# Kernel optimization log

Measured on AMD Instinct MI355X. Metric: run time of the kernel, lower is better.

## Reference

```python
import jax, jax.numpy as jnp
import numpy as np

L, H, N = 4096, 256, 64  # seq_len, hidden_size, hippo_n
EPS = 1e-5


def setup_inputs() -> dict:
    key = jax.random.key(0)
    ks = jax.random.split(key, 8)
    x = jax.random.normal(ks[0], (L, H), jnp.float32)
    # S4D-Lin style initialization for the diagonal SSM (H independent SSMs of state size N)
    Lambda_re = -0.5 * jnp.ones((H, N), jnp.float32)
    Lambda_im = jnp.tile(jnp.pi * jnp.arange(N, dtype=jnp.float32), (H, 1))
    B_re = jnp.ones((H, N), jnp.float32)
    B_im = jnp.zeros((H, N), jnp.float32)
    C_re = jax.random.normal(ks[1], (H, N), jnp.float32) * (0.5 ** 0.5)
    C_im = jax.random.normal(ks[2], (H, N), jnp.float32) * (0.5 ** 0.5)
    D = jax.random.normal(ks[3], (H,), jnp.float32)
    log_step = jax.random.uniform(ks[4], (H,), jnp.float32,
                                  minval=jnp.log(0.001), maxval=jnp.log(0.1))
    ln_w = jnp.ones((H,), jnp.float32)
    ln_b = jnp.zeros((H,), jnp.float32)
    sc = 1.0 / jnp.sqrt(jnp.float32(H))
    W1 = jax.random.normal(ks[5], (H, H), jnp.float32) * sc
    b1 = jnp.zeros((H,), jnp.float32)
    W2 = jax.random.normal(ks[6], (H, H), jnp.float32) * sc
    b2 = jnp.zeros((H,), jnp.float32)
    return {"x": x, "Lambda_re": Lambda_re, "Lambda_im": Lambda_im,
            "B_re": B_re, "B_im": B_im, "C_re": C_re, "C_im": C_im,
            "D": D, "log_step": log_step, "ln_w": ln_w, "ln_b": ln_b,
            "W1": W1, "b1": b1, "W2": W2, "b2": b2}


def reference(x, Lambda_re, Lambda_im, B_re, B_im, C_re, C_im, D, log_step,
              ln_w, ln_b, W1, b1, W2, b2):
    skip = x
    # per-token LayerNorm over the H feature axis (eqx.nn.LayerNorm, eps=1e-5)
    mu = jnp.mean(x, axis=-1, keepdims=True)
    var = jnp.mean(jnp.square(x - mu), axis=-1, keepdims=True)
    xn = (x - mu) / jnp.sqrt(var + EPS) * ln_w + ln_b  # [L, H]

    # ZOH discretization of the diagonal SSM (the cell.ssm(L) step)
    Lam = Lambda_re + 1j * Lambda_im                     # [H, N] complex64
    dt = jnp.exp(log_step)[:, None]                      # [H, 1]
    Ab = jnp.exp(Lam * dt)                               # [H, N]
    Bb = (Ab - 1.0) / Lam * (B_re + 1j * B_im)           # [H, N]
    C = C_re + 1j * C_im                                 # [H, N]

    def step(s, u):  # s: [H, N] complex state, u: [H] input at one time step
        s = Ab * s + Bb * u[:, None]
        y = 2.0 * jnp.einsum('hn,hn->h', C, s).real + D * u
        return s, y

    s0 = jnp.zeros((H, N), jnp.complex64)
    hidden, ys = jax.lax.scan(step, s0, xn)              # ys: [L, H]

    g = jax.nn.gelu(ys)
    out = (g @ W1.T + b1) * jax.nn.sigmoid(g @ W2.T + b2)  # GLU epilogue
    return (hidden, skip + out)
```

## Files before the change

### kernel.cpp

```cpp
#include <hip/hip_runtime.h>
#include <hip/hip_bf16.h>

#define LSEQ 4096
#define HDIM 256
#define NS   64
#define PC   32
#define MC   128

typedef __attribute__((ext_vector_type(8))) short short8;
typedef __attribute__((ext_vector_type(4))) float floatx4;

__global__ __launch_bounds__(256) void k_ln_stats(const float* __restrict__ x,
                                                  float* __restrict__ mu,
                                                  float* __restrict__ rstd) {
    int l = blockIdx.x, t = threadIdx.x;
    float v = x[l * HDIM + t];
    float s = v, s2 = v * v;
#pragma unroll
    for (int o = 32; o; o >>= 1) {
        s  += __shfl_xor(s, o);
        s2 += __shfl_xor(s2, o);
    }
    __shared__ float ps[4], ps2[4];
    int w = t >> 6;
    if ((t & 63) == 0) { ps[w] = s; ps2[w] = s2; }
    __syncthreads();
    if (t == 0) {
        float S = ps[0] + ps[1] + ps[2] + ps[3];
        float S2 = ps2[0] + ps2[1] + ps2[2] + ps2[3];
        float m = S * (1.0f / HDIM);
        float var = S2 * (1.0f / HDIM) - m * m;
        mu[l] = m;
        rstd[l] = rsqrtf(var + 1e-5f);
    }
}

__global__ __launch_bounds__(256) void k_transnorm(const float* __restrict__ x,
                                                   const float* __restrict__ mu,
                                                   const float* __restrict__ rstd,
                                                   const float* __restrict__ w,
                                                   const float* __restrict__ b,
                                                   float* __restrict__ xnT) {
    __shared__ float tile[64 * 65];
    int l0 = blockIdx.x * 64, h0 = blockIdx.y * 64;
    int t = threadIdx.x;
#pragma unroll
    for (int i = 0; i < 16; ++i) {
        int e = i * 256 + t;
        int r = e >> 6, c = e & 63;
        int l = l0 + r, h = h0 + c;
        float v = x[l * HDIM + h];
        v = (v - mu[l]) * rstd[l] * w[h] + b[h];
        tile[c * 65 + r] = v;
    }
    __syncthreads();
#pragma unroll
    for (int i = 0; i < 16; ++i) {
        int e = i * 256 + t;
        int hh = e >> 6, ll = e & 63;
        xnT[(size_t)(h0 + hh) * LSEQ + l0 + ll] = tile[hh * 65 + ll];
    }
}

__global__ __launch_bounds__(256) void k_wconv(const float* __restrict__ W1,
                                               const float* __restrict__ W2,
                                               unsigned short* __restrict__ w1b,
                                               unsigned short* __restrict__ w2b) {
    int g = blockIdx.x * 256 + threadIdx.x;
    float4 a = ((const float4*)W1)[g];
    float4 c = ((const float4*)W2)[g];
    ushort4 o1, o2;
    __hip_bfloat16 h;
    h = __float2bfloat16(a.x); o1.x = *(unsigned short*)&h;
    h = __float2bfloat16(a.y); o1.y = *(unsigned short*)&h;
    h = __float2bfloat16(a.z); o1.z = *(unsigned short*)&h;
    h = __float2bfloat16(a.w); o1.w = *(unsigned short*)&h;
    h = __float2bfloat16(c.x); o2.x = *(unsigned short*)&h;
    h = __float2bfloat16(c.y); o2.y = *(unsigned short*)&h;
    h = __float2bfloat16(c.z); o2.z = *(unsigned short*)&h;
    h = __float2bfloat16(c.w); o2.w = *(unsigned short*)&h;
    ((ushort4*)w1b)[g] = o1;
    ((ushort4*)w2b)[g] = o2;
}

__device__ inline void ssm_consts(const float* Lre, const float* Lim,
                                  const float* Bre, const float* Bim,
                                  const float* lstep, int h, int n,
                                  float& are, float& aim, float& bre, float& bim) {
    int idx = h * NS + n;
    float lre = Lre[idx], lim = Lim[idx];
    float dt = expf(lstep[h]);
    float er = expf(lre * dt);
    float sa, ca;
    sincosf(lim * dt, &sa, &ca);
    are = er * ca; aim = er * sa;
    float inv = 1.0f / (lre * lre + lim * lim);
    float nre = are - 1.0f, nim = aim;
    float tre = (nre * lre + nim * lim) * inv;
    float tim = (nim * lre - nre * lim) * inv;
    float br = Bre[idx], bi = Bim[idx];
    bre = tre * br - tim * bi;
    bim = tre * bi + tim * br;
}

__global__ __launch_bounds__(256) void k_scan_local(const float* __restrict__ xnT,
                                                    const float* __restrict__ Lre,
                                                    const float* __restrict__ Lim,
                                                    const float* __restrict__ Bre,
                                                    const float* __restrict__ Bim,
                                                    const float* __restrict__ lstep,
                                                    float2* __restrict__ f) {
    int wv = __builtin_amdgcn_readfirstlane((int)threadIdx.x) >> 6;
    int n = threadIdx.x & 63;
    int c = blockIdx.x * 4 + wv, h = blockIdx.y;
    const float* u = xnT + (size_t)h * LSEQ + c * MC;
    float are, aim, bre, bim;
    ssm_consts(Lre, Lim, Bre, Bim, lstep, h, n, are, aim, bre, bim);
    float sre = 0.f, sim = 0.f;
#pragma unroll 8
    for (int j = 0; j < MC; ++j) {
        float uv = u[j];
        float nr = fmaf(are, sre, fmaf(-aim, sim, bre * uv));
        float ni = fmaf(are, sim, fmaf( aim, sre, bim * uv));
        sre = nr; sim = ni;
    }
    f[(size_t)(h * PC + c) * NS + n] = make_float2(sre, sim);
}

__global__ __launch_bounds__(256) void k_scan_chunks(const float* __restrict__ Lre,
                                                     const float* __restrict__ Lim,
                                                     const float* __restrict__ lstep,
                                                     const float2* __restrict__ f,
                                                     float2* __restrict__ s0,
                                                     float* __restrict__ hid,
                                                     int interleaved) {
    int gid = blockIdx.x * 256 + threadIdx.x;
    int h = gid >> 6;
    float lre = Lre[gid], lim = Lim[gid];
    float dt = expf(lstep[h]);
    float er = expf(lre * dt);
    float sa, ca;
    sincosf(lim * dt, &sa, &ca);
    float ar = er * ca, ai = er * sa;
#pragma unroll
    for (int q = 0; q < 7; ++q) {
        float r2 = ar * ar - ai * ai;
        ai = 2.f * ar * ai;
        ar = r2;
    }
    float sre = 0.f, sim = 0.f;
#pragma unroll
    for (int c = 0; c < PC; ++c) {
        size_t idx = (size_t)(h * PC + c) * NS + (gid & 63);
        s0[idx] = make_float2(sre, sim);
        float2 fc = f[idx];
        float nr = fmaf(ar, sre, fmaf(-ai, sim, fc.x));
        float ni = fmaf(ar, sim, fmaf( ai, sre, fc.y));
        sre = nr; sim = ni;
    }
    if (interleaved) {
        ((float2*)hid)[gid] = make_float2(sre, sim);
    } else {
        hid[gid] = sre;
    }
}

__global__ __launch_bounds__(256) void k_scan_out(const float* __restrict__ xnT,
                                                  const float* __restrict__ Lre,
                                                  const float* __restrict__ Lim,
                                                  const float* __restrict__ Bre,
                                                  const float* __restrict__ Bim,
                                                  const float* __restrict__ Cre,
                                                  const float* __restrict__ Cim,
                                                  const float* __restrict__ Dv,
                                                  const float* __restrict__ lstep,
                                                  const float2* __restrict__ s0,
                                                  __hip_bfloat16* __restrict__ gb) {
    __shared__ __align__(16) float red[4][16 * 68];
    int wv = __builtin_amdgcn_readfirstlane((int)threadIdx.x) >> 6;
    int lane = threadIdx.x & 63;
    int c = blockIdx.x * 4 + wv, h = blockIdx.y, n = lane;
    const float* u = xnT + (size_t)h * LSEQ + c * MC;
    float are, aim, bre, bim;
    ssm_consts(Lre, Lim, Bre, Bim, lstep, h, n, are, aim, bre, bim);
    int idx = h * NS + n;
    float cre = Cre[idx], cim = Cim[idx];
    float Dh = Dv[h];
    float2 s00 = s0[(size_t)(h * PC + c) * NS + n];
    float sre = s00.x, sim = s00.y;

    float* rw = red[wv];
    int t16 = lane & 15, p = lane >> 4;

    for (int jg = 0; jg < 8; ++jg) {
#pragma unroll
        for (int tt = 0; tt < 16; ++tt) {
            float uv = u[jg * 16 + tt];
            float nr = fmaf(are, sre, fmaf(-aim, sim, bre * uv));
            float ni = fmaf(are, sim, fmaf( aim, sre, bim * uv));
            sre = nr; sim = ni;
            rw[tt * 68 + n] = fmaf(cre, sre, -(cim * sim));
        }
        float a0 = 0.f;
        const float4* rp = (const float4*)(rw + t16 * 68 + p * 16);
#pragma unroll
        for (int qq = 0; qq < 4; ++qq) {
            float4 v = rp[qq];
            a0 += (v.x + v.y) + (v.z + v.w);
        }
        a0 += __shfl_xor(a0, 16);
        a0 += __shfl_xor(a0, 32);
        if (lane < 16) {
            int l = c * MC + jg * 16 + t16;
            float uv2 = u[jg * 16 + t16];
            float y = fmaf(2.f, a0, Dh * uv2);
            float z = 0.7978845608028654f * fmaf(0.044715f, y * y * y, y);
            float e = __expf(2.f * z);
            float th = 1.f - 2.f / (e + 1.f);
            float g = 0.5f * y * (1.f + th);
            gb[(size_t)l * HDIM + h] = __float2bfloat16(g);
        }
    }
}

__global__ __launch_bounds__(64) void k_glu_mfma(const unsigned short* __restrict__ gbs,
                                                 const unsigned short* __restrict__ w1b,
                                                 const unsigned short* __restrict__ w2b,
                                                 const float* __restrict__ b1v,
                                                 const float* __restrict__ b2v,
                                                 const float* __restrict__ x,
                                                 float* __restrict__ out) {
    int bx = blockIdx.x;
    int m0 = (bx >> 3) * 32;
    int n0 = (bx & 7) * 32;
    int lane = threadIdx.x;
    int t = lane & 15, q = lane >> 4;

    floatx4 acc[2][2][2];
#pragma unroll
    for (int a = 0; a < 2; ++a)
#pragma unroll
        for (int b = 0; b < 2; ++b)
#pragma unroll
            for (int g = 0; g < 2; ++g)
                acc[a][b][g] = (floatx4){0.f, 0.f, 0.f, 0.f};

    const unsigned short* A0  = gbs + (size_t)(m0 + t) * HDIM + q * 8;
    const unsigned short* A1  = A0 + 16 * HDIM;
    const unsigned short* B10 = w1b + (size_t)(n0 + t) * HDIM + q * 8;
    const unsigned short* B11 = B10 + 16 * HDIM;
    const unsigned short* B20 = w2b + (size_t)(n0 + t) * HDIM + q * 8;
    const unsigned short* B21 = B20 + 16 * HDIM;

#pragma unroll
    for (int ks = 0; ks < 8; ++ks) {
        int off = ks * 32;
        short8 a0  = *(const short8*)(A0  + off);
        short8 a1  = *(const short8*)(A1  + off);
        short8 b10 = *(const short8*)(B10 + off);
        short8 b11 = *(const short8*)(B11 + off);
        short8 b20 = *(const short8*)(B20 + off);
        short8 b21 = *(const short8*)(B21 + off);
        acc[0][0][0] = __builtin_amdgcn_mfma_f32_16x16x32_bf16(a0, b10, acc[0][0][0], 0, 0, 0);
        acc[0][1][0] = __builtin_amdgcn_mfma_f32_16x16x32_bf16(a0, b11, acc[0][1][0], 0, 0, 0);
        acc[1][0][0] = __builtin_amdgcn_mfma_f32_16x16x32_bf16(a1, b10, acc[1][0][0], 0, 0, 0);
        acc[1][1][0] = __builtin_amdgcn_mfma_f32_16x16x32_bf16(a1, b11, acc[1][1][0], 0, 0, 0);
        acc[0][0][1] = __builtin_amdgcn_mfma_f32_16x16x32_bf16(a0, b20, acc[0][0][1], 0, 0, 0);
        acc[0][1][1] = __builtin_amdgcn_mfma_f32_16x16x32_bf16(a0, b21, acc[0][1][1], 0, 0, 0);
        acc[1][0][1] = __builtin_amdgcn_mfma_f32_16x16x32_bf16(a1, b20, acc[1][0][1], 0, 0, 0);
        acc[1][1][1] = __builtin_amdgcn_mfma_f32_16x16x32_bf16(a1, b21, acc[1][1][1], 0, 0, 0);
    }

#pragma unroll
    for (int nt = 0; nt < 2; ++nt) {
        int hh = n0 + nt * 16 + t;
        float bb1 = b1v[hh], bb2 = b2v[hh];
#pragma unroll
        for (int mt = 0; mt < 2; ++mt) {
#pragma unroll
            for (int reg = 0; reg < 4; ++reg) {
                int l = m0 + mt * 16 + q * 4 + reg;
                float a  = acc[mt][nt][0][reg] + bb1;
                float sg = 1.f / (1.f + __expf(-(acc[mt][nt][1][reg] + bb2)));
                out[(size_t)l * HDIM + hh] = fmaf(a, sg, x[(size_t)l * HDIM + hh]);
            }
        }
    }
}

extern "C" void kernel_launch(void* const* d_in, const int* in_sizes, int n_in,
                              void* d_out, int out_size, void* d_ws, size_t ws_size,
                              hipStream_t stream) {
    (void)in_sizes; (void)n_in; (void)ws_size;
    const float* x     = (const float*)d_in[0];
    const float* Lre   = (const float*)d_in[1];
    const float* Lim   = (const float*)d_in[2];
    const float* Bre   = (const float*)d_in[3];
    const float* Bim   = (const float*)d_in[4];
    const float* Cre   = (const float*)d_in[5];
    const float* Cim   = (const float*)d_in[6];
    const float* Dv    = (const float*)d_in[7];
    const float* lstep = (const float*)d_in[8];
    const float* lnw   = (const float*)d_in[9];
    const float* lnb   = (const float*)d_in[10];
    const float* W1    = (const float*)d_in[11];
    const float* b1    = (const float*)d_in[12];
    const float* W2    = (const float*)d_in[13];
    const float* b2    = (const float*)d_in[14];

    float* ws   = (float*)d_ws;
    float* mu   = ws;
    float* rstd = ws + LSEQ;
    float* xnT  = ws + 2 * LSEQ;
    float2* f   = (float2*)(xnT + (size_t)HDIM * LSEQ);
    float2* s0  = f + (size_t)HDIM * PC * NS;
    unsigned short* gb  = (unsigned short*)(s0 + (size_t)HDIM * PC * NS);
    unsigned short* w1b = gb + (size_t)LSEQ * HDIM;
    unsigned short* w2b = w1b + HDIM * HDIM;

    int interleaved = (out_size == LSEQ * HDIM + 2 * HDIM * NS) ? 1 : 0;
    float* hid  = (float*)d_out;
    float* outp = (float*)d_out + (interleaved ? 2 * HDIM * NS : HDIM * NS);

    k_ln_stats   <<<LSEQ, 256, 0, stream>>>(x, mu, rstd);
    k_transnorm  <<<dim3(LSEQ / 64, HDIM / 64), 256, 0, stream>>>(x, mu, rstd, lnw, lnb, xnT);
    k_wconv      <<<64, 256, 0, stream>>>(W1, W2, w1b, w2b);
    k_scan_local <<<dim3(PC / 4, HDIM), 256, 0, stream>>>(xnT, Lre, Lim, Bre, Bim, lstep, f);
    k_scan_chunks<<<(HDIM * NS) / 256, 256, 0, stream>>>(Lre, Lim, lstep, f, s0, hid, interleaved);
    k_scan_out   <<<dim3(PC / 4, HDIM), 256, 0, stream>>>(xnT, Lre, Lim, Bre, Bim, Cre, Cim,
                                                          Dv, lstep, s0, (__hip_bfloat16*)gb);
    k_glu_mfma   <<<128 * 8, 64, 0, stream>>>(gb, w1b, w2b, b1, b2, x, outp);
}
```

Measured before the change: 135.1 us.

## Fuse chunk-carry scan into output scan, merge weight conversion, broadcast inputs via readlane

Drops the separate chunk-prefix kernel: each wave of the output scan now rebuilds its own starting state by folding the chunk-final states of all earlier chunks with A^128, and the last chunk writes the hidden state. The bf16 weight conversion moves into extra blocks of the LN-stats kernel, so there are two fewer launches. Both scan kernels now load 64 inputs with one coalesced per-lane load and broadcast each one with readlane, replacing repeated scalar loads. The cost is redundant prefix work that grows with the chunk index (up to 31 steps), plus the loss of the s0 buffer.

```diff
diff --git a/kernel.cpp b/kernel.cpp
--- a/kernel.cpp
+++ b/kernel.cpp
@@ -10,10 +10,37 @@
 typedef __attribute__((ext_vector_type(8))) short short8;
 typedef __attribute__((ext_vector_type(4))) float floatx4;
 
+__device__ __forceinline__ float lane_bcast(float v, int j) {
+    return __uint_as_float(__builtin_amdgcn_readlane(__float_as_uint(v), j));
+}
+
 __global__ __launch_bounds__(256) void k_ln_stats(const float* __restrict__ x,
                                                   float* __restrict__ mu,
-                                                  float* __restrict__ rstd) {
-    int l = blockIdx.x, t = threadIdx.x;
+                                                  float* __restrict__ rstd,
+                                                  const float* __restrict__ W1,
+                                                  const float* __restrict__ W2,
+                                                  unsigned short* __restrict__ w1b,
+                                                  unsigned short* __restrict__ w2b) {
+    int t = threadIdx.x;
+    if (blockIdx.x >= LSEQ) {
+        int g = (blockIdx.x - LSEQ) * 256 + t;
+        float4 a = ((const float4*)W1)[g];
+        float4 c = ((const float4*)W2)[g];
+        ushort4 o1, o2;
+        __hip_bfloat16 h;
+        h = __float2bfloat16(a.x); o1.x = *(unsigned short*)&h;
+        h = __float2bfloat16(a.y); o1.y = *(unsigned short*)&h;
+        h = __float2bfloat16(a.z); o1.z = *(unsigned short*)&h;
+        h = __float2bfloat16(a.w); o1.w = *(unsigned short*)&h;
+        h = __float2bfloat16(c.x); o2.x = *(unsigned short*)&h;
+        h = __float2bfloat16(c.y); o2.y = *(unsigned short*)&h;
+        h = __float2bfloat16(c.z); o2.z = *(unsigned short*)&h;
+        h = __float2bfloat16(c.w); o2.w = *(unsigned short*)&h;
+        ((ushort4*)w1b)[g] = o1;
+        ((ushort4*)w2b)[g] = o2;
+        return;
+    }
+    int l = blockIdx.x;
     float v = x[l * HDIM + t];
     float s = v, s2 = v * v;
 #pragma unroll
@@ -60,27 +87,6 @@
         int hh = e >> 6, ll = e & 63;
         xnT[(size_t)(h0 + hh) * LSEQ + l0 + ll] = tile[hh * 65 + ll];
     }
-}
-
-__global__ __launch_bounds__(256) void k_wconv(const float* __restrict__ W1,
-                                               const float* __restrict__ W2,
-                                               unsigned short* __restrict__ w1b,
-                                               unsigned short* __restrict__ w2b) {
-    int g = blockIdx.x * 256 + threadIdx.x;
-    float4 a = ((const float4*)W1)[g];
-    float4 c = ((const float4*)W2)[g];
-    ushort4 o1, o2;
-    __hip_bfloat16 h;
-    h = __float2bfloat16(a.x); o1.x = *(unsigned short*)&h;
-    h = __float2bfloat16(a.y); o1.y = *(unsigned short*)&h;
-    h = __float2bfloat16(a.z); o1.z = *(unsigned short*)&h;
-    h = __float2bfloat16(a.w); o1.w = *(unsigned short*)&h;
-    h = __float2bfloat16(c.x); o2.x = *(unsigned short*)&h;
-    h = __float2bfloat16(c.y); o2.y = *(unsigned short*)&h;
-    h = __float2bfloat16(c.z); o2.z = *(unsigned short*)&h;
-    h = __float2bfloat16(c.w); o2.w = *(unsigned short*)&h;
-    ((ushort4*)w1b)[g] = o1;
-    ((ushort4*)w2b)[g] = o2;
 }
 
 __device__ inline void ssm_consts(const float* Lre, const float* Lim,
@@ -117,52 +123,17 @@
     float are, aim, bre, bim;
     ssm_consts(Lre, Lim, Bre, Bim, lstep, h, n, are, aim, bre, bim);
     float sre = 0.f, sim = 0.f;
-#pragma unroll 8
-    for (int j = 0; j < MC; ++j) {
-        float uv = u[j];
-        float nr = fmaf(are, sre, fmaf(-aim, sim, bre * uv));
-        float ni = fmaf(are, sim, fmaf( aim, sre, bim * uv));
-        sre = nr; sim = ni;
+    for (int g = 0; g < 2; ++g) {
+        float uv = u[g * 64 + n];
+#pragma unroll
+        for (int j = 0; j < 64; ++j) {
+            float us = lane_bcast(uv, j);
+            float nr = fmaf(are, sre, fmaf(-aim, sim, bre * us));
+            float ni = fmaf(are, sim, fmaf( aim, sre, bim * us));
+            sre = nr; sim = ni;
+        }
     }
     f[(size_t)(h * PC + c) * NS + n] = make_float2(sre, sim);
-}
-
-__global__ __launch_bounds__(256) void k_scan_chunks(const float* __restrict__ Lre,
-                                                     const float* __restrict__ Lim,
-                                                     const float* __restrict__ lstep,
-                                                     const float2* __restrict__ f,
-                                                     float2* __restrict__ s0,
-                                                     float* __restrict__ hid,
-                                                     int interleaved) {
-    int gid = blockIdx.x * 256 + threadIdx.x;
-    int h = gid >> 6;
-    float lre = Lre[gid], lim = Lim[gid];
-    float dt = expf(lstep[h]);
-    float er = expf(lre * dt);
-    float sa, ca;
-    sincosf(lim * dt, &sa, &ca);
-    float ar = er * ca, ai = er * sa;
-#pragma unroll
-    for (int q = 0; q < 7; ++q) {
-        float r2 = ar * ar - ai * ai;
-        ai = 2.f * ar * ai;
-        ar = r2;
-    }
-    float sre = 0.f, sim = 0.f;
-#pragma unroll
-    for (int c = 0; c < PC; ++c) {
-        size_t idx = (size_t)(h * PC + c) * NS + (gid & 63);
-        s0[idx] = make_float2(sre, sim);
-        float2 fc = f[idx];
-        float nr = fmaf(ar, sre, fmaf(-ai, sim, fc.x));
-        float ni = fmaf(ar, sim, fmaf( ai, sre, fc.y));
-        sre = nr; sim = ni;
-    }
-    if (interleaved) {
-        ((float2*)hid)[gid] = make_float2(sre, sim);
-    } else {
-        hid[gid] = sre;
-    }
 }
 
 __global__ __launch_bounds__(256) void k_scan_out(const float* __restrict__ xnT,
@@ -174,8 +145,10 @@
                                                   const float* __restrict__ Cim,
                                                   const float* __restrict__ Dv,
                                                   const float* __restrict__ lstep,
-                                                  const float2* __restrict__ s0,
-                                                  __hip_bfloat16* __restrict__ gb) {
+                                                  const float2* __restrict__ f,
+                                                  __hip_bfloat16* __restrict__ gb,
+                                                  float* __restrict__ hid,
+                                                  int interleaved) {
     __shared__ __align__(16) float red[4][16 * 68];
     int wv = __builtin_amdgcn_readfirstlane((int)threadIdx.x) >> 6;
     int lane = threadIdx.x & 63;
@@ -186,39 +159,64 @@
     int idx = h * NS + n;
     float cre = Cre[idx], cim = Cim[idx];
     float Dh = Dv[h];
-    float2 s00 = s0[(size_t)(h * PC + c) * NS + n];
-    float sre = s00.x, sim = s00.y;
+
+    float ar = are, ai = aim;
+#pragma unroll
+    for (int q = 0; q < 7; ++q) {
+        float r2 = ar * ar - ai * ai;
+        ai = 2.f * ar * ai;
+        ar = r2;
+    }
+    float sre = 0.f, sim = 0.f;
+    for (int cp = 0; cp < c; ++cp) {
+        float2 fc = f[(size_t)(h * PC + cp) * NS + n];
+        float nr = fmaf(ar, sre, fmaf(-ai, sim, fc.x));
+        float ni = fmaf(ar, sim, fmaf( ai, sre, fc.y));
+        sre = nr; sim = ni;
+    }
 
     float* rw = red[wv];
     int t16 = lane & 15, p = lane >> 4;
 
-    for (int jg = 0; jg < 8; ++jg) {
-#pragma unroll
-        for (int tt = 0; tt < 16; ++tt) {
-            float uv = u[jg * 16 + tt];
-            float nr = fmaf(are, sre, fmaf(-aim, sim, bre * uv));
-            float ni = fmaf(are, sim, fmaf( aim, sre, bim * uv));
-            sre = nr; sim = ni;
-            rw[tt * 68 + n] = fmaf(cre, sre, -(cim * sim));
+    for (int g = 0; g < 2; ++g) {
+        float uv = u[g * 64 + lane];
+#pragma unroll
+        for (int jg = 0; jg < 4; ++jg) {
+#pragma unroll
+            for (int tt = 0; tt < 16; ++tt) {
+                float us = lane_bcast(uv, jg * 16 + tt);
+                float nr = fmaf(are, sre, fmaf(-aim, sim, bre * us));
+                float ni = fmaf(are, sim, fmaf( aim, sre, bim * us));
+                sre = nr; sim = ni;
+                rw[tt * 68 + n] = fmaf(cre, sre, -(cim * sim));
+            }
+            float a0 = 0.f;
+            const float4* rp = (const float4*)(rw + t16 * 68 + p * 16);
+#pragma unroll
+            for (int qq = 0; qq < 4; ++qq) {
+                float4 v = rp[qq];
+                a0 += (v.x + v.y) + (v.z + v.w);
+            }
+            a0 += __shfl_xor(a0, 16);
+            a0 += __shfl_xor(a0, 32);
+            float u_tok = __shfl(uv, jg * 16 + t16);
+            if (lane < 16) {
+                int l = c * MC + g * 64 + jg * 16 + t16;
+                float y = fmaf(2.f, a0, Dh * u_tok);
+                float z = 0.7978845608028654f * fmaf(0.044715f, y * y * y, y);
+                float e = __expf(2.f * z);
+                float th = 1.f - 2.f / (e + 1.f);
+                float gg = 0.5f * y * (1.f + th);
+                gb[(size_t)l * HDIM + h] = __float2bfloat16(gg);
+            }
         }
-        float a0 = 0.f;
-        const float4* rp = (const float4*)(rw + t16 * 68 + p * 16);
-#pragma unroll
-        for (int qq = 0; qq < 4; ++qq) {
-            float4 v = rp[qq];
-            a0 += (v.x + v.y) + (v.z + v.w);
-        }
-        a0 += __shfl_xor(a0, 16);
-        a0 += __shfl_xor(a0, 32);
-        if (lane < 16) {
-            int l = c * MC + jg * 16 + t16;
-            float uv2 = u[jg * 16 + t16];
-            float y = fmaf(2.f, a0, Dh * uv2);
-            float z = 0.7978845608028654f * fmaf(0.044715f, y * y * y, y);
-            float e = __expf(2.f * z);
-            float th = 1.f - 2.f / (e + 1.f);
-            float g = 0.5f * y * (1.f + th);
-            gb[(size_t)l * HDIM + h] = __float2bfloat16(g);
+    }
+
+    if (c == PC - 1) {
+        if (interleaved) {
+            ((float2*)hid)[idx] = make_float2(sre, sim);
+        } else {
+            hid[idx] = sre;
         }
     }
 }
@@ -313,8 +311,7 @@
     float* rstd = ws + LSEQ;
     float* xnT  = ws + 2 * LSEQ;
     float2* f   = (float2*)(xnT + (size_t)HDIM * LSEQ);
-    float2* s0  = f + (size_t)HDIM * PC * NS;
-    unsigned short* gb  = (unsigned short*)(s0 + (size_t)HDIM * PC * NS);
+    unsigned short* gb  = (unsigned short*)(f + (size_t)HDIM * PC * NS);
     unsigned short* w1b = gb + (size_t)LSEQ * HDIM;
     unsigned short* w2b = w1b + HDIM * HDIM;
 
@@ -322,12 +319,11 @@
     float* hid  = (float*)d_out;
     float* outp = (float*)d_out + (interleaved ? 2 * HDIM * NS : HDIM * NS);
 
-    k_ln_stats   <<<LSEQ, 256, 0, stream>>>(x, mu, rstd);
+    k_ln_stats   <<<LSEQ + 64, 256, 0, stream>>>(x, mu, rstd, W1, W2, w1b, w2b);
     k_transnorm  <<<dim3(LSEQ / 64, HDIM / 64), 256, 0, stream>>>(x, mu, rstd, lnw, lnb, xnT);
-    k_wconv      <<<64, 256, 0, stream>>>(W1, W2, w1b, w2b);
     k_scan_local <<<dim3(PC / 4, HDIM), 256, 0, stream>>>(xnT, Lre, Lim, Bre, Bim, lstep, f);
-    k_scan_chunks<<<(HDIM * NS) / 256, 256, 0, stream>>>(Lre, Lim, lstep, f, s0, hid, interleaved);
     k_scan_out   <<<dim3(PC / 4, HDIM), 256, 0, stream>>>(xnT, Lre, Lim, Bre, Bim, Cre, Cim,
-                                                          Dv, lstep, s0, (__hip_bfloat16*)gb);
+                                                          Dv, lstep, f, (__hip_bfloat16*)gb,
+                                                          hid, interleaved);
     k_glu_mfma   <<<128 * 8, 64, 0, stream>>>(gb, w1b, w2b, b1, b2, x, outp);
 }
```

Result: slower. 139.0 us (+2.9%).
